# Optimization experiments

Measured on AMD Instinct MI355X. Metric: run time of the kernel, lower is better.

Reference implementation:

```python
import jax, jax.numpy as jnp
import numpy as np

B, S, E, H = 4, 2048, 1024, 16
D = E // H  # head_dim = 64


def setup_inputs() -> dict:
    key = jax.random.key(0)
    ks = jax.random.split(key, 7)
    scale = 1.0 / np.sqrt(E)
    inp = {
        "query": jax.random.normal(ks[0], (B, S, E), jnp.float32),
        "key": jax.random.normal(ks[1], (B, S, E), jnp.float32),
        "value": jax.random.normal(ks[2], (B, S, E), jnp.float32),
        # nn.Linear weights: [out_features, in_features]
        "Wq": jax.random.normal(ks[3], (E, E), jnp.float32) * scale,
        "Wk": jax.random.normal(ks[4], (E, E), jnp.float32) * scale,
        "Wv": jax.random.normal(ks[5], (E, E), jnp.float32) * scale,
        "Wo": jax.random.normal(ks[6], (E, E), jnp.float32) * scale,
        # broadcastable causal mask; masked_fill where mask == 0
        "mask": jnp.tril(jnp.ones((S, S), jnp.bool_))[None, None, :, :],
    }
    return inp


def reference(query, key, value, Wq, Wk, Wv, Wo, mask):
    # projections (Linear, no bias): x @ W.T
    Q = (query @ Wq.T).reshape(B, S, H, D)
    K = (key @ Wk.T).reshape(B, S, H, D)
    V = (value @ Wv.T).reshape(B, S, H, D)
    # full score matrix [B,H,S,S]
    scores = jnp.einsum("bqhd,bkhd->bhqk", Q, K) / jnp.sqrt(jnp.float32(D))
    scores = jnp.where(mask, scores, jnp.float32(-1e20))
    attn = jax.nn.softmax(scores, axis=-1)
    out = jnp.einsum("bhqk,bkhd->bqhd", attn, V).reshape(B, S, E)
    return out @ Wo.T
```

## Files before the change

kernel.cpp:

```cpp
#include <hip/hip_runtime.h>
#include <stdint.h>


#define LOG2E 1.44269504088896340736f

typedef __bf16 bf16;
typedef __attribute__((ext_vector_type(8))) __bf16 bf16x8;
typedef __attribute__((ext_vector_type(4))) __bf16 bf16x4;
typedef __attribute__((ext_vector_type(4))) float f32x4;

static constexpr int Sq = 2048, Eq = 1024;

__device__ __forceinline__ f32x4 mfma16(bf16x8 a, bf16x8 b, f32x4 c) {
  return __builtin_amdgcn_mfma_f32_16x16x32_bf16(a, b, c, 0, 0, 0);
}

__device__ __forceinline__ float fexp2(float x) {
  return __builtin_amdgcn_exp2f(x);
}

__device__ __forceinline__ void gload16(const bf16* g, bf16* l) {
  __builtin_amdgcn_global_load_lds(
      (const __attribute__((address_space(1))) void*)g,
      (__attribute__((address_space(3))) void*)l, 16, 0, 0);
}

__device__ __forceinline__ bf16x8 scale8(bf16x8 v, float s) {
  bf16x8 o;
#pragma unroll
  for (int i = 0; i < 8; ++i) o[i] = (bf16)((float)v[i] * s);
  return o;
}

__device__ __forceinline__ void store4(bf16* p, f32x4 a, float s) {
  bf16x4 v;
#pragma unroll
  for (int rg = 0; rg < 4; ++rg) v[rg] = (bf16)(a[rg] * s);
  *(bf16x4*)p = v;
}

__device__ __forceinline__ bf16x8 cvt8(const float4& a, const float4& b) {
  bf16x8 v;
  v[0] = (bf16)a.x; v[1] = (bf16)a.y; v[2] = (bf16)a.z; v[3] = (bf16)a.w;
  v[4] = (bf16)b.x; v[5] = (bf16)b.y; v[6] = (bf16)b.z; v[7] = (bf16)b.w;
  return v;
}

__global__ void cast_w4(const float* __restrict__ a, const float* __restrict__ b,
                        const float* __restrict__ c, const float* __restrict__ d,
                        bf16* __restrict__ oa, bf16* __restrict__ ob,
                        bf16* __restrict__ oc, bf16* __restrict__ od) {
  int i = blockIdx.x * blockDim.x + threadIdx.x;
  int sel = i >> 17, off = i & ((1 << 17) - 1);
  const float* src = sel == 0 ? a : sel == 1 ? b : sel == 2 ? c : d;
  bf16* dst = sel == 0 ? oa : sel == 1 ? ob : sel == 2 ? oc : od;
  const float4* p = (const float4*)src;
  ((bf16x8*)dst)[off] = cvt8(p[off * 2], p[off * 2 + 1]);
}

template <int MODE>
__global__ __launch_bounds__(256) void gemm_proj(const float* __restrict__ Af,
                                                 const bf16* __restrict__ W,
                                                 bf16* __restrict__ C) {
  __shared__ __align__(16) bf16 Alds[128 * 64];
  __shared__ __align__(16) bf16 Blds[128 * 64];

  int bid = blockIdx.x;
  int wg = (bid & 7) * 64 + (bid >> 3);
  int tm = wg >> 3, tn = wg & 7;
  int tid = threadIdx.x;
  int l = tid & 63, wv = tid >> 6;
  int wm = wv >> 1, wn = wv & 1;
  int l15 = l & 15, lg = l >> 4;

  f32x4 acc[4][4] = {};
  const size_t arow = (size_t)tm * 128, brow = (size_t)tn * 128;

  for (int k0 = 0; k0 < 1024; k0 += 64) {
#pragma unroll
    for (int j = 0; j < 4; ++j) {
      int loc = tid * 16 + j * 4096;
      int r = loc >> 7;
      int c = (loc & 127) >> 1;
      gload16(W + (brow + r) * 1024 + k0 + c, (bf16*)((char*)Blds + loc));
    }
#pragma unroll
    for (int j = 0; j < 4; ++j) {
      int row = (tid >> 3) + j * 32;
      int colf = (tid & 7) * 8;
      const float4* ap = (const float4*)(Af + (arow + row) * 1024 + k0 + colf);
      float4 a0 = ap[0], a1 = ap[1];
      *(bf16x8*)(Alds + row * 64 + colf) = cvt8(a0, a1);
    }
    __syncthreads();
#pragma unroll
    for (int kk = 0; kk < 2; ++kk) {
      bf16x8 af[4], bfr[4];
#pragma unroll
      for (int t = 0; t < 4; ++t) {
        int ma = wm * 64 + t * 16 + l15;
        af[t] = *(const bf16x8*)((const char*)Alds + ma * 128 + 16 * lg + 64 * kk);
        int nb = wn * 64 + t * 16 + l15;
        bfr[t] = *(const bf16x8*)((const char*)Blds + nb * 128 + 16 * lg + 64 * kk);
      }
#pragma unroll
      for (int mt = 0; mt < 4; ++mt)
#pragma unroll
        for (int nt = 0; nt < 4; ++nt)
          acc[mt][nt] = mfma16(af[mt], bfr[nt], acc[mt][nt]);
    }
    __syncthreads();
  }

  int mbase = tm * 128 + wm * 64;
  int nbase = tn * 128 + wn * 64;
  if (MODE == 0) {
#pragma unroll
    for (int mt = 0; mt < 4; ++mt)
#pragma unroll
      for (int nt = 0; nt < 4; ++nt) {
        int m0 = mbase + mt * 16 + (lg << 2);
        int n = nbase + nt * 16 + l15;
#pragma unroll
        for (int rg = 0; rg < 4; ++rg)
          C[(size_t)(m0 + rg) * 1024 + n] = (bf16)acc[mt][nt][rg];
      }
  } else {
#pragma unroll
    for (int mt = 0; mt < 4; ++mt)
#pragma unroll
      for (int nt = 0; nt < 4; ++nt) {
        int m0 = mbase + mt * 16 + (lg << 2);
        int n = nbase + nt * 16 + l15;
        bf16x4 vv;
#pragma unroll
        for (int rg = 0; rg < 4; ++rg) vv[rg] = (bf16)acc[mt][nt][rg];
        int bb = m0 >> 11, s0 = m0 & 2047;
        int sp = (s0 & ~31) | (((s0 >> 4) & 1) << 2) | (((s0 >> 2) & 3) << 3);
        size_t off =
            ((size_t)((bb * 16 + (n >> 6)) * 64 + (n & 63))) * 2048 + sp;
        *(bf16x4*)(C + off) = vv;
      }
  }
}

__global__ __launch_bounds__(256) void gemm_wo(const bf16* __restrict__ A,
                                               const bf16* __restrict__ W,
                                               float* __restrict__ Cout) {
  __shared__ __align__(16) bf16 Alds[128 * 64];
  __shared__ __align__(16) bf16 Blds[128 * 64];

  int bid = blockIdx.x;
  int wg = (bid & 7) * 64 + (bid >> 3);
  int tm = wg >> 3, tn = wg & 7;
  int tid = threadIdx.x;
  int l = tid & 63, wv = tid >> 6;
  int wm = wv >> 1, wn = wv & 1;
  int l15 = l & 15, lg = l >> 4;

  f32x4 acc[4][4] = {};
  const size_t arow = (size_t)tm * 128, brow = (size_t)tn * 128;

  for (int k0 = 0; k0 < 1024; k0 += 64) {
#pragma unroll
    for (int j = 0; j < 4; ++j) {
      int loc = tid * 16 + j * 4096;
      int r = loc >> 7;
      int c = (loc & 127) >> 1;
      gload16(W + (brow + r) * 1024 + k0 + c, (bf16*)((char*)Blds + loc));
      gload16(A + (arow + r) * 1024 + k0 + c, (bf16*)((char*)Alds + loc));
    }
    __syncthreads();
#pragma unroll
    for (int kk = 0; kk < 2; ++kk) {
      bf16x8 af[4], bfr[4];
#pragma unroll
      for (int t = 0; t < 4; ++t) {
        int ma = wm * 64 + t * 16 + l15;
        af[t] = *(const bf16x8*)((const char*)Alds + ma * 128 + 16 * lg + 64 * kk);
        int nb = wn * 64 + t * 16 + l15;
        bfr[t] = *(const bf16x8*)((const char*)Blds + nb * 128 + 16 * lg + 64 * kk);
      }
#pragma unroll
      for (int mt = 0; mt < 4; ++mt)
#pragma unroll
        for (int nt = 0; nt < 4; ++nt)
          acc[mt][nt] = mfma16(af[mt], bfr[nt], acc[mt][nt]);
    }
    __syncthreads();
  }

  int mbase = tm * 128 + wm * 64;
  int nbase = tn * 128 + wn * 64;
#pragma unroll
  for (int mt = 0; mt < 4; ++mt)
#pragma unroll
    for (int nt = 0; nt < 4; ++nt) {
      int m0 = mbase + mt * 16 + (lg << 2);
      int n = nbase + nt * 16 + l15;
#pragma unroll
      for (int rg = 0; rg < 4; ++rg)
        Cout[(size_t)(m0 + rg) * 1024 + n] = acc[mt][nt][rg];
    }
}

__global__ __launch_bounds__(256) void attn_kernel(
    const bf16* __restrict__ Qp, const bf16* __restrict__ Kp,
    const bf16* __restrict__ Vt, bf16* __restrict__ AO) {
  __shared__ __align__(16) bf16 sm[3][2][4096];

  int bid = blockIdx.x;
  int bh = ((bid & 7) << 3) | ((bid >> 3) & 7);
  int j = bid >> 6;
  int b = bh >> 4, h = bh & 15;
  int tid = threadIdx.x;
  int w = tid >> 6, l = tid & 63;
  int l15 = l & 15, lg = l >> 4;

  const int ncA = 2 * j + 2;
  const int NC = 34;
  const float sc = 0.125f * LOG2E;
  bf16 one1 = (bf16)1.0f;
  bf16x8 ones = {one1, one1, one1, one1, one1, one1, one1, one1};

  const bf16* Kbase = Kp + (size_t)(b * 2048) * 1024 + h * 64;
  const bf16* Vbase = Vt + (size_t)(bh * 64) * 2048;

  int qw0 = j * 128 + w * 32;
  int cdiag = 2 * j + (w >> 1);
  int qg0 = qw0 + l15, qg1 = qw0 + 16 + l15;
  const bf16* qp_ = Qp + (size_t)(b * 2048 + qw0 + l15) * 1024 + h * 64 + 8 * lg;
  bf16x8 q00 = scale8(*(const bf16x8*)qp_, sc);
  bf16x8 q01 = scale8(*(const bf16x8*)(qp_ + 32), sc);
  bf16x8 q10 = scale8(*(const bf16x8*)(qp_ + 16384), sc);
  bf16x8 q11 = scale8(*(const bf16x8*)(qp_ + 16384 + 32), sc);

  f32x4 r0 = {0.f, 0.f, 0.f, 0.f}, r1 = r0;
  f32x4 o0[4] = {}, o1[4] = {};

#define STAGE(c_, bufp)                                                     \
  do {                                                                      \
    int _c = (c_);                                                          \
    _Pragma("unroll") for (int jj = 0; jj < 2; ++jj) {                      \
      int loc = tid * 16 + jj * 4096;                                       \
      int row = loc >> 7, u = (loc >> 4) & 7;                               \
      int sel = (u ^ (row & 7)) << 3;                                       \
      gload16(Kbase + (size_t)(_c * 64 + row) * 1024 + sel,                 \
              (bf16*)((char*)sm[bufp][0] + loc));                           \
      gload16(Vbase + (size_t)row * 2048 + _c * 64 + sel,                   \
              (bf16*)((char*)sm[bufp][1] + loc));                           \
    }                                                                       \
  } while (0)

#define CHUNKC(c_, bufc_)                                                   \
  do {                                                                      \
    const int _c = (c_);                                                    \
    const char* lK = (const char*)sm[bufc_][0];                             \
    const char* lV = (const char*)sm[bufc_][1];                             \
    const f32x4 cinit = {-6.f, -6.f, -6.f, -6.f};                           \
    f32x4 s0[4], s1[4];                                                     \
    _Pragma("unroll") for (int kt = 0; kt < 4; ++kt) {                      \
      int row = kt * 16 + l15, sw = (row & 7) << 4;                         \
      const char* kb = lK + row * 128;                                      \
      bf16x8 kf0 = *(const bf16x8*)(kb + ((lg * 16) ^ sw));                 \
      bf16x8 kf1 = *(const bf16x8*)(kb + ((64 + lg * 16) ^ sw));            \
      s0[kt] = mfma16(kf1, q01, mfma16(kf0, q00, cinit));                   \
      s1[kt] = mfma16(kf1, q11, mfma16(kf0, q10, cinit));                   \
    }                                                                       \
    if (_c == cdiag) {                                                      \
      _Pragma("unroll") for (int kt = 0; kt < 4; ++kt)                      \
          _Pragma("unroll") for (int rg = 0; rg < 4; ++rg) {                \
        int kg = _c * 64 + kt * 16 + 4 * lg + rg;                           \
        if (kg > qg0) s0[kt][rg] = -1e30f;                                  \
        if (kg > qg1) s1[kt][rg] = -1e30f;                                  \
      }                                                                     \
    }                                                                       \
    bf16x8 plo0, phi0, plo1, phi1;                                          \
    _Pragma("unroll") for (int rg = 0; rg < 4; ++rg) {                      \
      plo0[rg] = (bf16)fexp2(s0[0][rg]); plo0[rg + 4] = (bf16)fexp2(s0[1][rg]); \
      phi0[rg] = (bf16)fexp2(s0[2][rg]); phi0[rg + 4] = (bf16)fexp2(s0[3][rg]); \
      plo1[rg] = (bf16)fexp2(s1[0][rg]); plo1[rg + 4] = (bf16)fexp2(s1[1][rg]); \
      phi1[rg] = (bf16)fexp2(s1[2][rg]); phi1[rg + 4] = (bf16)fexp2(s1[3][rg]); \
    }                                                                       \
    r0 = mfma16(ones, phi0, mfma16(ones, plo0, r0));                        \
    r1 = mfma16(ones, phi1, mfma16(ones, plo1, r1));                        \
    _Pragma("unroll") for (int dt = 0; dt < 4; ++dt) {                      \
      int row = dt * 16 + l15, sw = (row & 7) << 4;                         \
      const char* vb = lV + row * 128;                                      \
      bf16x8 vf0 = *(const bf16x8*)(vb + ((lg * 16) ^ sw));                 \
      bf16x8 vf1 = *(const bf16x8*)(vb + ((64 + lg * 16) ^ sw));            \
      o0[dt] = mfma16(vf1, phi0, mfma16(vf0, plo0, o0[dt]));                \
      o1[dt] = mfma16(vf1, phi1, mfma16(vf0, plo1, o1[dt]));                \
    }                                                                       \
  } while (0)

#define STOREOUT()                                                          \
  do {                                                                      \
    float inv0 = 1.0f / r0[0], inv1 = 1.0f / r1[0];                         \
    bf16* ob = AO + (size_t)(b * 2048 + qw0 + l15) * 1024 + h * 64 + 4 * lg; \
    _Pragma("unroll") for (int dt = 0; dt < 4; ++dt) {                      \
      store4(ob + dt * 16, o0[dt], inv0);                                   \
      store4(ob + 16384 + dt * 16, o1[dt], inv1);                           \
    }                                                                       \
  } while (0)

  STAGE(0, 0);
  STAGE(1, 1);

  for (int g = 0; g < NC; ++g) {
    if (g < NC - 1)
      asm volatile("s_waitcnt vmcnt(4)\n\ts_barrier" ::: "memory");
    else
      asm volatile("s_waitcnt vmcnt(0)\n\ts_barrier" ::: "memory");

    if (g + 2 < NC) {
      int gn = g + 2;
      int cn = gn < ncA ? gn : gn - ncA;
      STAGE(cn, gn % 3);
    }

    if (g == ncA) {
      STOREOUT();
      qw0 = (15 - j) * 128 + w * 32;
      cdiag = 2 * (15 - j) + (w >> 1);
      qg0 = qw0 + l15; qg1 = qw0 + 16 + l15;
      qp_ = Qp + (size_t)(b * 2048 + qw0 + l15) * 1024 + h * 64 + 8 * lg;
      q00 = scale8(*(const bf16x8*)qp_, sc);
      q01 = scale8(*(const bf16x8*)(qp_ + 32), sc);
      q10 = scale8(*(const bf16x8*)(qp_ + 16384), sc);
      q11 = scale8(*(const bf16x8*)(qp_ + 16384 + 32), sc);
      r0 = f32x4{0.f, 0.f, 0.f, 0.f}; r1 = r0;
#pragma unroll
      for (int dt = 0; dt < 4; ++dt) { o0[dt] = r0; o1[dt] = r0; }
    }

    int c = g < ncA ? g : g - ncA;
    if (c <= cdiag) CHUNKC(c, g % 3);
  }
  STOREOUT();
#undef STAGE
#undef CHUNKC
#undef STOREOUT
}

extern "C" void kernel_launch(void* const* d_in, const int* in_sizes, int n_in,
                              void* d_out, int out_size, void* d_ws, size_t ws_size,
                              hipStream_t stream) {
  (void)in_sizes; (void)n_in; (void)out_size; (void)ws_size;
  const float* dq = (const float*)d_in[0];
  const float* dk = (const float*)d_in[1];
  const float* dv = (const float*)d_in[2];
  const float* wq = (const float*)d_in[3];
  const float* wk = (const float*)d_in[4];
  const float* wv = (const float*)d_in[5];
  const float* wo = (const float*)d_in[6];

  char* ws = (char*)d_ws;
  const size_t MB = 1u << 20;
  bf16* AO  = (bf16*)(ws + 0 * MB);
  bf16* wqb = (bf16*)(ws + 48 * MB);
  bf16* wkb = (bf16*)(ws + 50 * MB);
  bf16* wvb = (bf16*)(ws + 52 * MB);
  bf16* wob = (bf16*)(ws + 54 * MB);
  bf16* Qp  = (bf16*)(ws + 56 * MB);
  bf16* Kp  = (bf16*)(ws + 72 * MB);
  bf16* Vt  = (bf16*)(ws + 88 * MB);

  cast_w4<<<4 * 512, 256, 0, stream>>>(wq, wk, wv, wo, wqb, wkb, wvb, wob);
  gemm_proj<0><<<512, 256, 0, stream>>>(dq, wqb, Qp);
  gemm_proj<0><<<512, 256, 0, stream>>>(dk, wkb, Kp);
  gemm_proj<1><<<512, 256, 0, stream>>>(dv, wvb, Vt);
  attn_kernel<<<512, 256, 0, stream>>>(Qp, Kp, Vt, AO);
  gemm_wo<<<512, 256, 0, stream>>>(AO, wob, (float*)d_out);
}
```

Measured before the change: 190.7 us.

## Halve attention query tile to 64 rows, double grid, double-buffer K/V with setprio

The attention kernel now gives each block 64 query rows (16 per wave) instead of 128, paired as tiles t and 31-t for causal load balance, and launches 1024 blocks instead of 512. K/V staging goes from a triple-buffered vmcnt-based pipeline to a two-buffer scheme with a __syncthreads per chunk. MFMA sections are wrapped in s_setprio so waves can interleave compute with other waves' exp work. The aim is more parallelism and less LDS and register use per block, at the cost of half the K/V reuse per staged chunk, more global and LDS traffic, and a full barrier every iteration.

```diff
diff --git a/kernel.cpp b/kernel.cpp
--- a/kernel.cpp
+++ b/kernel.cpp
@@ -207,18 +207,18 @@
 __global__ __launch_bounds__(256) void attn_kernel(
     const bf16* __restrict__ Qp, const bf16* __restrict__ Kp,
     const bf16* __restrict__ Vt, bf16* __restrict__ AO) {
-  __shared__ __align__(16) bf16 sm[3][2][4096];
+  __shared__ __align__(16) bf16 sm[2][2][4096];
 
   int bid = blockIdx.x;
   int bh = ((bid & 7) << 3) | ((bid >> 3) & 7);
-  int j = bid >> 6;
+  int t = bid >> 6;
   int b = bh >> 4, h = bh & 15;
   int tid = threadIdx.x;
   int w = tid >> 6, l = tid & 63;
   int l15 = l & 15, lg = l >> 4;
 
-  const int ncA = 2 * j + 2;
-  const int NC = 34;
+  const int ncA = t + 1;
+  const int NC = 33;
   const float sc = 0.125f * LOG2E;
   bf16 one1 = (bf16)1.0f;
   bf16x8 ones = {one1, one1, one1, one1, one1, one1, one1, one1};
@@ -226,17 +226,13 @@
   const bf16* Kbase = Kp + (size_t)(b * 2048) * 1024 + h * 64;
   const bf16* Vbase = Vt + (size_t)(bh * 64) * 2048;
 
-  int qw0 = j * 128 + w * 32;
-  int cdiag = 2 * j + (w >> 1);
-  int qg0 = qw0 + l15, qg1 = qw0 + 16 + l15;
+  int qw0 = 64 * t + w * 16;
+  int qg0 = qw0 + l15;
   const bf16* qp_ = Qp + (size_t)(b * 2048 + qw0 + l15) * 1024 + h * 64 + 8 * lg;
   bf16x8 q00 = scale8(*(const bf16x8*)qp_, sc);
   bf16x8 q01 = scale8(*(const bf16x8*)(qp_ + 32), sc);
-  bf16x8 q10 = scale8(*(const bf16x8*)(qp_ + 16384), sc);
-  bf16x8 q11 = scale8(*(const bf16x8*)(qp_ + 16384 + 32), sc);
-
-  f32x4 r0 = {0.f, 0.f, 0.f, 0.f}, r1 = r0;
-  f32x4 o0[4] = {}, o1[4] = {};
+  f32x4 r0 = {0.f, 0.f, 0.f, 0.f};
+  f32x4 o0[4] = {};
 
 #define STAGE(c_, bufp)                                                     \
   do {                                                                      \
@@ -252,90 +248,81 @@
     }                                                                       \
   } while (0)
 
-#define CHUNKC(c_, bufc_)                                                   \
+#define CHUNKC(c_, last_)                                                   \
   do {                                                                      \
     const int _c = (c_);                                                    \
-    const char* lK = (const char*)sm[bufc_][0];                             \
-    const char* lV = (const char*)sm[bufc_][1];                             \
+    const char* lK = (const char*)sm[cur][0];                               \
+    const char* lV = (const char*)sm[cur][1];                               \
     const f32x4 cinit = {-6.f, -6.f, -6.f, -6.f};                           \
-    f32x4 s0[4], s1[4];                                                     \
+    f32x4 s[4];                                                             \
+    __builtin_amdgcn_s_setprio(1);                                          \
     _Pragma("unroll") for (int kt = 0; kt < 4; ++kt) {                      \
       int row = kt * 16 + l15, sw = (row & 7) << 4;                         \
       const char* kb = lK + row * 128;                                      \
       bf16x8 kf0 = *(const bf16x8*)(kb + ((lg * 16) ^ sw));                 \
       bf16x8 kf1 = *(const bf16x8*)(kb + ((64 + lg * 16) ^ sw));            \
-      s0[kt] = mfma16(kf1, q01, mfma16(kf0, q00, cinit));                   \
-      s1[kt] = mfma16(kf1, q11, mfma16(kf0, q10, cinit));                   \
-    }                                                                       \
-    if (_c == cdiag) {                                                      \
+      s[kt] = mfma16(kf1, q01, mfma16(kf0, q00, cinit));                    \
+    }                                                                       \
+    __builtin_amdgcn_s_setprio(0);                                          \
+    if (last_) {                                                            \
       _Pragma("unroll") for (int kt = 0; kt < 4; ++kt)                      \
           _Pragma("unroll") for (int rg = 0; rg < 4; ++rg) {                \
         int kg = _c * 64 + kt * 16 + 4 * lg + rg;                           \
-        if (kg > qg0) s0[kt][rg] = -1e30f;                                  \
-        if (kg > qg1) s1[kt][rg] = -1e30f;                                  \
+        if (kg > qg0) s[kt][rg] = -1e30f;                                   \
       }                                                                     \
     }                                                                       \
-    bf16x8 plo0, phi0, plo1, phi1;                                          \
+    bf16x8 plo, phi;                                                        \
     _Pragma("unroll") for (int rg = 0; rg < 4; ++rg) {                      \
-      plo0[rg] = (bf16)fexp2(s0[0][rg]); plo0[rg + 4] = (bf16)fexp2(s0[1][rg]); \
-      phi0[rg] = (bf16)fexp2(s0[2][rg]); phi0[rg + 4] = (bf16)fexp2(s0[3][rg]); \
-      plo1[rg] = (bf16)fexp2(s1[0][rg]); plo1[rg + 4] = (bf16)fexp2(s1[1][rg]); \
-      phi1[rg] = (bf16)fexp2(s1[2][rg]); phi1[rg + 4] = (bf16)fexp2(s1[3][rg]); \
-    }                                                                       \
-    r0 = mfma16(ones, phi0, mfma16(ones, plo0, r0));                        \
-    r1 = mfma16(ones, phi1, mfma16(ones, plo1, r1));                        \
+      plo[rg] = (bf16)fexp2(s[0][rg]);                                      \
+      plo[rg + 4] = (bf16)fexp2(s[1][rg]);                                  \
+      phi[rg] = (bf16)fexp2(s[2][rg]);                                      \
+      phi[rg + 4] = (bf16)fexp2(s[3][rg]);                                  \
+    }                                                                       \
+    __builtin_amdgcn_s_setprio(1);                                          \
+    r0 = mfma16(ones, phi, mfma16(ones, plo, r0));                          \
     _Pragma("unroll") for (int dt = 0; dt < 4; ++dt) {                      \
       int row = dt * 16 + l15, sw = (row & 7) << 4;                         \
       const char* vb = lV + row * 128;                                      \
       bf16x8 vf0 = *(const bf16x8*)(vb + ((lg * 16) ^ sw));                 \
       bf16x8 vf1 = *(const bf16x8*)(vb + ((64 + lg * 16) ^ sw));            \
-      o0[dt] = mfma16(vf1, phi0, mfma16(vf0, plo0, o0[dt]));                \
-      o1[dt] = mfma16(vf1, phi1, mfma16(vf0, plo1, o1[dt]));                \
-    }                                                                       \
+      o0[dt] = mfma16(vf1, phi, mfma16(vf0, plo, o0[dt]));                  \
+    }                                                                       \
+    __builtin_amdgcn_s_setprio(0);                                          \
   } while (0)
 
 #define STOREOUT()                                                          \
   do {                                                                      \
-    float inv0 = 1.0f / r0[0], inv1 = 1.0f / r1[0];                         \
+    float inv = 1.0f / r0[0];                                               \
     bf16* ob = AO + (size_t)(b * 2048 + qw0 + l15) * 1024 + h * 64 + 4 * lg; \
-    _Pragma("unroll") for (int dt = 0; dt < 4; ++dt) {                      \
-      store4(ob + dt * 16, o0[dt], inv0);                                   \
-      store4(ob + 16384 + dt * 16, o1[dt], inv1);                           \
-    }                                                                       \
+    _Pragma("unroll") for (int dt = 0; dt < 4; ++dt)                        \
+        store4(ob + dt * 16, o0[dt], inv);                                  \
   } while (0)
 
   STAGE(0, 0);
-  STAGE(1, 1);
+  __syncthreads();
+  int cur = 0;
 
   for (int g = 0; g < NC; ++g) {
-    if (g < NC - 1)
-      asm volatile("s_waitcnt vmcnt(4)\n\ts_barrier" ::: "memory");
-    else
-      asm volatile("s_waitcnt vmcnt(0)\n\ts_barrier" ::: "memory");
-
-    if (g + 2 < NC) {
-      int gn = g + 2;
-      int cn = gn < ncA ? gn : gn - ncA;
-      STAGE(cn, gn % 3);
-    }
-
+    if (g + 1 < NC) {
+      int gn = g + 1;
+      STAGE(gn < ncA ? gn : gn - ncA, cur ^ 1);
+    }
     if (g == ncA) {
       STOREOUT();
-      qw0 = (15 - j) * 128 + w * 32;
-      cdiag = 2 * (15 - j) + (w >> 1);
-      qg0 = qw0 + l15; qg1 = qw0 + 16 + l15;
+      qw0 = 64 * (31 - t) + w * 16;
+      qg0 = qw0 + l15;
       qp_ = Qp + (size_t)(b * 2048 + qw0 + l15) * 1024 + h * 64 + 8 * lg;
       q00 = scale8(*(const bf16x8*)qp_, sc);
       q01 = scale8(*(const bf16x8*)(qp_ + 32), sc);
-      q10 = scale8(*(const bf16x8*)(qp_ + 16384), sc);
-      q11 = scale8(*(const bf16x8*)(qp_ + 16384 + 32), sc);
-      r0 = f32x4{0.f, 0.f, 0.f, 0.f}; r1 = r0;
-#pragma unroll
-      for (int dt = 0; dt < 4; ++dt) { o0[dt] = r0; o1[dt] = r0; }
-    }
-
+      r0 = f32x4{0.f, 0.f, 0.f, 0.f};
+#pragma unroll
+      for (int dt = 0; dt < 4; ++dt) o0[dt] = r0;
+    }
     int c = g < ncA ? g : g - ncA;
-    if (c <= cdiag) CHUNKC(c, g % 3);
+    bool last = (g == ncA - 1) || (g == NC - 1);
+    CHUNKC(c, last);
+    __syncthreads();
+    cur ^= 1;
   }
   STOREOUT();
 #undef STAGE
@@ -370,6 +357,6 @@
   gemm_proj<0><<<512, 256, 0, stream>>>(dq, wqb, Qp);
   gemm_proj<0><<<512, 256, 0, stream>>>(dk, wkb, Kp);
   gemm_proj<1><<<512, 256, 0, stream>>>(dv, wvb, Vt);
-  attn_kernel<<<512, 256, 0, stream>>>(Qp, Kp, Vt, AO);
+  attn_kernel<<<1024, 256, 0, stream>>>(Qp, Kp, Vt, AO);
   gemm_wo<<<512, 256, 0, stream>>>(AO, wob, (float*)d_out);
 }
```

Result: faster. 186.6 us (-2.2%).
